# Kernel optimization log

Measured on AMD Instinct MI355X. Metric: run time of the kernel, lower is better.

Reference implementation:

```python
import jax, jax.numpy as jnp
import numpy as np

B, C, N = 8, 256, 2048

def setup_inputs() -> dict:
    key = jax.random.key(0)
    ks = jax.random.split(key, 7)
    s = 1.0 / np.sqrt(C)
    return {
        "x": jax.random.normal(ks[0], (B, C, N), dtype=jnp.float32),
        "Wq": jax.random.normal(ks[1], (C, C), dtype=jnp.float32) * s,
        "bq": jax.random.normal(ks[2], (C,), dtype=jnp.float32) * s,
        "Wk": jax.random.normal(ks[3], (C, C), dtype=jnp.float32) * s,
        "bk": jax.random.normal(ks[4], (C,), dtype=jnp.float32) * s,
        "Wv": jax.random.normal(ks[5], (C, C), dtype=jnp.float32) * s,
        "bv": jax.random.normal(ks[6], (C,), dtype=jnp.float32) * s,
    }

def reference(x, Wq, bq, Wk, bk, Wv, bv):
    # x: [B, C, N]; Conv1d(k=1) == channel-mixing matmul + bias
    q = jnp.einsum('oc,bcn->bon', Wq, x) + bq[None, :, None]  # [B,C,N]
    k = jnp.einsum('oc,bcn->bon', Wk, x) + bk[None, :, None]  # [B,C,N]
    v = jnp.einsum('oc,bcn->bon', Wv, x) + bv[None, :, None]  # [B,C,N]
    # qk = bmm(q^T, k): [B, N, N]
    qk = jnp.einsum('bcn,bcm->bnm', q, k)
    # global-sum normalization over the ENTIRE qk tensor (not row-wise softmax)
    attn_w = qk / jnp.sum(qk)
    # attn = bmm(v, attn_w): [B, C, N]
    attn = jnp.einsum('bcn,bnm->bcm', v, attn_w)
    return attn
```

## Files before the change

### kernel.cpp

```cpp
#include <hip/hip_runtime.h>


typedef _Float16 half8 __attribute__((ext_vector_type(8)));
typedef _Float16 half4 __attribute__((ext_vector_type(4)));
typedef _Float16 half2v __attribute__((ext_vector_type(2)));
typedef float f4v __attribute__((ext_vector_type(4)));

#define GP  40
#define GPB 36

__launch_bounds__(256)
__global__ void k1_kernel(const float* __restrict__ x, const float* __restrict__ Wq,
                          const float* __restrict__ Wk, const float* __restrict__ bq,
                          const float* __restrict__ bk, float* __restrict__ sxpart,
                          float* __restrict__ W3, float* __restrict__ u2,
                          float* __restrict__ w1, float* __restrict__ s1,
                          float* __restrict__ S, float* __restrict__ Gpart) {
    __shared__ __align__(16) char smem[40960];
    const int blk = blockIdx.x, t = threadIdx.x;
    if (blk < 192) {
        _Float16* Ah = (_Float16*)smem;
        _Float16* Al = Ah + 128 * GP;
        _Float16* Bh = Al + 128 * GP;
        _Float16* Bl = Bh + 128 * GP;
        const int tileId = blk % 3;
        const int y = blk / 3;
        const int b = y >> 3, ks = y & 7;
        const int r0 = (tileId == 2) ? 128 : 0;
        const int c0 = (tileId == 0) ? 0 : 128;
        const bool diag = (tileId != 1);
        const float* xb = x + (long)b * 524288;

        const int lane = t & 63, wave = t >> 6;
        const int wy = wave >> 1, wx = wave & 1;
        const int mIn = lane & 15, quad = lane >> 4;

        f4v acc[4][4] = {};
        const int aBase = (wy * 64 + mIn) * GP + quad * 8;
        const int bBase = (wx * 64 + mIn) * GP + quad * 8;
        const int srow = t >> 3;
        const int skq  = (t & 7) * 4;
        float rs[4] = {};

        float4 pa[4], pb[4];
        int kk = ks * 256;
        #pragma unroll
        for (int i = 0; i < 4; ++i) {
            pa[i] = *(const float4*)&xb[(long)(r0 + srow + i * 32) * 2048 + kk + skq];
            if (!diag) pb[i] = *(const float4*)&xb[(long)(c0 + srow + i * 32) * 2048 + kk + skq];
        }

        for (int kb = 0; kb < 8; ++kb) {
            if (kb) __syncthreads();
            #pragma unroll
            for (int i = 0; i < 4; ++i) {
                const int row = srow + i * 32;
                half4 hv, lv;
                hv[0] = (_Float16)pa[i].x; lv[0] = (_Float16)(pa[i].x - (float)hv[0]);
                hv[1] = (_Float16)pa[i].y; lv[1] = (_Float16)(pa[i].y - (float)hv[1]);
                hv[2] = (_Float16)pa[i].z; lv[2] = (_Float16)(pa[i].z - (float)hv[2]);
                hv[3] = (_Float16)pa[i].w; lv[3] = (_Float16)(pa[i].w - (float)hv[3]);
                *(half4*)&Ah[row * GP + skq] = hv;
                *(half4*)&Al[row * GP + skq] = lv;
                if (diag) {
                    rs[i] += pa[i].x + pa[i].y + pa[i].z + pa[i].w;
                } else {
                    half4 hb, lb;
                    hb[0] = (_Float16)pb[i].x; lb[0] = (_Float16)(pb[i].x - (float)hb[0]);
                    hb[1] = (_Float16)pb[i].y; lb[1] = (_Float16)(pb[i].y - (float)hb[1]);
                    hb[2] = (_Float16)pb[i].z; lb[2] = (_Float16)(pb[i].z - (float)hb[2]);
                    hb[3] = (_Float16)pb[i].w; lb[3] = (_Float16)(pb[i].w - (float)hb[3]);
                    *(half4*)&Bh[row * GP + skq] = hb;
                    *(half4*)&Bl[row * GP + skq] = lb;
                }
            }
            __syncthreads();
            kk += 32;
            if (kb < 7) {
                #pragma unroll
                for (int i = 0; i < 4; ++i) {
                    pa[i] = *(const float4*)&xb[(long)(r0 + srow + i * 32) * 2048 + kk + skq];
                    if (!diag) pb[i] = *(const float4*)&xb[(long)(c0 + srow + i * 32) * 2048 + kk + skq];
                }
            }
            const _Float16* BhP = diag ? Ah : Bh;
            const _Float16* BlP = diag ? Al : Bl;
            #pragma unroll
            for (int ph = 0; ph < 3; ++ph) {
                const _Float16* As = (ph == 2) ? Al : Ah;
                const _Float16* Bs = (ph == 1) ? BlP : BhP;
                half8 af[4], bf[4];
                #pragma unroll
                for (int i = 0; i < 4; ++i) {
                    af[i] = *(const half8*)&As[aBase + i * 16 * GP];
                    bf[i] = *(const half8*)&Bs[bBase + i * 16 * GP];
                }
                #pragma unroll
                for (int i = 0; i < 4; ++i)
                    #pragma unroll
                    for (int j = 0; j < 4; ++j)
                        acc[i][j] = __builtin_amdgcn_mfma_f32_16x16x32_f16(af[i], bf[j], acc[i][j], 0, 0, 0);
            }
        }

        if (diag) {
            #pragma unroll
            for (int i = 0; i < 4; ++i) {
                rs[i] += __shfl_xor(rs[i], 1);
                rs[i] += __shfl_xor(rs[i], 2);
                rs[i] += __shfl_xor(rs[i], 4);
            }
            if ((t & 7) == 0) {
                #pragma unroll
                for (int i = 0; i < 4; ++i)
                    sxpart[ks * 2048 + b * 256 + r0 + srow + i * 32] = rs[i];
            }
        }

        float* D = Gpart + ((long)(ks * 8 + b) << 16);
        #pragma unroll
        for (int i = 0; i < 4; ++i)
            #pragma unroll
            for (int j = 0; j < 4; ++j) {
                const int row = r0 + wy * 64 + i * 16 + quad * 4;
                const int col = c0 + wx * 64 + j * 16 + mIn;
                #pragma unroll
                for (int r = 0; r < 4; ++r)
                    D[(row + r) * 256 + col] = acc[i][j][r];
                if (tileId == 1)
                    *(float4*)&D[(long)col * 256 + row] =
                        make_float4(acc[i][j][0], acc[i][j][1], acc[i][j][2], acc[i][j][3]);
            }
    } else if (blk < 208) {
        float* ldsA = (float*)smem;
        float* ldsB = ldsA + 16 * 68;
        const int tile = blk - 192;
        const int r0 = (tile >> 2) * 64, j0 = (tile & 3) * 64;
        const int tx = t & 15, ty = t >> 4;
        float acc[4][4] = {};
        for (int kk = 0; kk < 256; kk += 16) {
            *(float4*)&ldsA[ty * 68 + tx * 4] = *(const float4*)&Wq[(long)(kk + ty) * 256 + r0 + tx * 4];
            *(float4*)&ldsB[ty * 68 + tx * 4] = *(const float4*)&Wk[(long)(kk + ty) * 256 + j0 + tx * 4];
            __syncthreads();
            #pragma unroll
            for (int k = 0; k < 16; ++k) {
                const float4 av4 = *(const float4*)&ldsA[k * 68 + ty * 4];
                const float4 bv4 = *(const float4*)&ldsB[k * 68 + tx * 4];
                const float ar[4] = {av4.x, av4.y, av4.z, av4.w};
                const float br[4] = {bv4.x, bv4.y, bv4.z, bv4.w};
                #pragma unroll
                for (int i = 0; i < 4; ++i)
                    #pragma unroll
                    for (int j = 0; j < 4; ++j)
                        acc[i][j] = fmaf(ar[i], br[j], acc[i][j]);
            }
            __syncthreads();
        }
        #pragma unroll
        for (int i = 0; i < 4; ++i)
            *(float4*)&W3[(long)(r0 + ty * 4 + i) * 256 + j0 + tx * 4] =
                make_float4(acc[i][0], acc[i][1], acc[i][2], acc[i][3]);
    } else {
        float* sbq = (float*)smem;
        float* sbk = sbq + 256;
        float* red = sbk + 256;
        if (t == 0) S[0] = 0.0f;
        sbq[t] = bq[t]; sbk[t] = bk[t];
        __syncthreads();
        float u = 0.0f, w = 0.0f;
        #pragma unroll 8
        for (int c = 0; c < 256; ++c) {
            u = fmaf(Wk[(long)c * 256 + t], sbq[c], u);
            w = fmaf(Wq[(long)c * 256 + t], sbk[c], w);
        }
        u2[t] = u; w1[t] = w;
        red[t] = sbq[t] * sbk[t]; __syncthreads();
        for (int h = 128; h > 0; h >>= 1) { if (t < h) red[t] += red[t + h]; __syncthreads(); }
        if (t == 0) s1[0] = red[0];
    }
}

__launch_bounds__(256)
__global__ void k2_kernel(const float* __restrict__ Wv, const float* __restrict__ Gpart,
                          const float* __restrict__ W3, const float* __restrict__ u2,
                          const float* __restrict__ w1, const float* __restrict__ s1p,
                          const float* __restrict__ sxpart, float* __restrict__ T1,
                          float* __restrict__ v2, float* __restrict__ s2,
                          float* __restrict__ wvsx, float* __restrict__ S) {
    __shared__ __align__(16) char smem[40960];
    const int blk = blockIdx.x, t = threadIdx.x;
    if (blk < 128) {
        float* ldsA = (float*)smem;
        float* ldsB = ldsA + 16 * 68;
        const int j0 = (blk & 3) * 64;
        const int r0 = ((blk >> 2) & 3) * 64;
        const int b = blk >> 4;
        const int tx = t & 15, ty = t >> 4;
        const int sr = t >> 2, sk = (t & 3) * 4;
        float acc[4][4] = {};
        for (int kk = 0; kk < 256; kk += 16) {
            const float4 a4 = *(const float4*)&Wv[(long)(r0 + sr) * 256 + kk + sk];
            ldsA[(sk + 0) * 68 + sr] = a4.x;
            ldsA[(sk + 1) * 68 + sr] = a4.y;
            ldsA[(sk + 2) * 68 + sr] = a4.z;
            ldsA[(sk + 3) * 68 + sr] = a4.w;
            float4 bs = make_float4(0.f, 0.f, 0.f, 0.f);
            #pragma unroll
            for (int ksl = 0; ksl < 8; ++ksl) {
                const float4 g = *(const float4*)&Gpart[(long)ksl * 524288 + (long)b * 65536 +
                                                        (long)(kk + ty) * 256 + j0 + tx * 4];
                bs.x += g.x; bs.y += g.y; bs.z += g.z; bs.w += g.w;
            }
            *(float4*)&ldsB[ty * 68 + tx * 4] = bs;
            __syncthreads();
            #pragma unroll
            for (int k = 0; k < 16; ++k) {
                const float4 av4 = *(const float4*)&ldsA[k * 68 + ty * 4];
                const float4 bv4 = *(const float4*)&ldsB[k * 68 + tx * 4];
                const float ar[4] = {av4.x, av4.y, av4.z, av4.w};
                const float br[4] = {bv4.x, bv4.y, bv4.z, bv4.w};
                #pragma unroll
                for (int i = 0; i < 4; ++i)
                    #pragma unroll
                    for (int j = 0; j < 4; ++j)
                        acc[i][j] = fmaf(ar[i], br[j], acc[i][j]);
            }
            __syncthreads();
        }
        float* D = T1 + (long)b * 65536;
        #pragma unroll
        for (int i = 0; i < 4; ++i)
            *(float4*)&D[(long)(r0 + ty * 4 + i) * 256 + j0 + tx * 4] =
                make_float4(acc[i][0], acc[i][1], acc[i][2], acc[i][3]);
    } else if (blk < 136) {
        float* ssx = (float*)smem;
        float* red = ssx + 256;
        const int b = blk - 128, j = t;
        float sxv = 0.0f;
        #pragma unroll
        for (int ks = 0; ks < 8; ++ks) sxv += sxpart[ks * 2048 + b * 256 + j];
        ssx[j] = sxv;
        __syncthreads();
        float vr = 0.0f;
        #pragma unroll 8
        for (int c = 0; c < 256; ++c) vr = fmaf(W3[(long)c * 256 + j], ssx[c], vr);
        const float v2j = vr + 2048.0f * u2[j];
        v2[b * 256 + j] = v2j;
        red[j] = v2j * sxv; __syncthreads();
        for (int h = 128; h > 0; h >>= 1) { if (j < h) red[j] += red[j + h]; __syncthreads(); }
        const float sd1 = red[0];
        __syncthreads();
        red[j] = sxv * w1[j]; __syncthreads();
        for (int h = 128; h > 0; h >>= 1) { if (j < h) red[j] += red[j + h]; __syncthreads(); }
        if (j == 0) {
            const float s2v = red[0] + 2048.0f * s1p[0];
            s2[b] = s2v;
            atomicAdd(S, sd1 + 2048.0f * s2v);
        }
    } else {
        float* wtile = (float*)smem;
        float* sxs = wtile + 8192;
        const int r0w = (blk - 136) * 32;
        #pragma unroll
        for (int p = 0; p < 8; ++p) {
            const int f = t + p * 256;
            const int row = f >> 6, c4 = f & 63;
            *(float4*)&wtile[row * 256 + c4 * 4] = *(const float4*)&Wv[(long)(r0w + row) * 256 + c4 * 4];
        }
        #pragma unroll
        for (int p = 0; p < 8; ++p) {
            const int f = t + p * 256;
            float s = 0.0f;
            #pragma unroll
            for (int ks = 0; ks < 8; ++ks) s += sxpart[ks * 2048 + f];
            sxs[f] = s;
        }
        __syncthreads();
        const int r = t >> 3, q = t & 7;
        float acc[8] = {};
        for (int ci = 0; ci < 32; ++ci) {
            const float wv = wtile[r * 256 + q * 32 + ci];
            #pragma unroll
            for (int b = 0; b < 8; ++b) acc[b] = fmaf(wv, sxs[b * 256 + q * 32 + ci], acc[b]);
        }
        #pragma unroll
        for (int b = 0; b < 8; ++b) {
            acc[b] += __shfl_xor(acc[b], 1);
            acc[b] += __shfl_xor(acc[b], 2);
            acc[b] += __shfl_xor(acc[b], 4);
        }
        if (q == 0) {
            #pragma unroll
            for (int b = 0; b < 8; ++b) wvsx[b * 256 + r0w + r] = acc[b];
        }
    }
}

__launch_bounds__(256)
__global__ void ap_kernel(const float* __restrict__ T1, const float* __restrict__ W3,
                          const float* __restrict__ wvsx, const float* __restrict__ u2,
                          const float* __restrict__ bv, const float* __restrict__ v2,
                          const float* __restrict__ w1, const float* __restrict__ s1p,
                          const float* __restrict__ s2, _Float16* __restrict__ Aph,
                          _Float16* __restrict__ Apl, float* __restrict__ cvec) {
    __shared__ float ldsA[16 * 68], ldsB[16 * 68], sw1[256];
    const int b = blockIdx.z;
    const int r0 = blockIdx.y * 64, j0 = blockIdx.x * 64;
    const float* A = T1 + (long)b * 65536;
    const int t = threadIdx.x, tx = t & 15, ty = t >> 4;
    const int sr = t >> 2, sk = (t & 3) * 4;
    sw1[t] = w1[t];
    float acc[4][4] = {};
    float dot[4] = {};
    for (int kk = 0; kk < 256; kk += 16) {
        const float4 a4 = *(const float4*)&A[(long)(r0 + sr) * 256 + kk + sk];
        ldsA[(sk + 0) * 68 + sr] = a4.x;
        ldsA[(sk + 1) * 68 + sr] = a4.y;
        ldsA[(sk + 2) * 68 + sr] = a4.z;
        ldsA[(sk + 3) * 68 + sr] = a4.w;
        *(float4*)&ldsB[ty * 68 + tx * 4] = *(const float4*)&W3[(long)(kk + ty) * 256 + j0 + tx * 4];
        __syncthreads();
        #pragma unroll
        for (int k = 0; k < 16; ++k) {
            const float4 av4 = *(const float4*)&ldsA[k * 68 + ty * 4];
            const float4 bv4 = *(const float4*)&ldsB[k * 68 + tx * 4];
            const float ar[4] = {av4.x, av4.y, av4.z, av4.w};
            const float br[4] = {bv4.x, bv4.y, bv4.z, bv4.w};
            const float wk = sw1[kk + k];
            #pragma unroll
            for (int i = 0; i < 4; ++i) {
                dot[i] = fmaf(ar[i], wk, dot[i]);
                #pragma unroll
                for (int j = 0; j < 4; ++j)
                    acc[i][j] = fmaf(ar[i], br[j], acc[i][j]);
            }
        }
        __syncthreads();
    }
    #pragma unroll
    for (int i = 0; i < 4; ++i) {
        const int r = r0 + ty * 4 + i;
        const float e1 = wvsx[b * 256 + r], e3 = bv[r];
        half4 hv, lv;
        #pragma unroll
        for (int j = 0; j < 4; ++j) {
            const int col = j0 + tx * 4 + j;
            const float val = acc[i][j] + e1 * u2[col] + e3 * v2[b * 256 + col];
            hv[j] = (_Float16)val;
            lv[j] = (_Float16)(val - (float)hv[j]);
        }
        const long o = (long)b * 65536 + (long)r * 256 + j0 + tx * 4;
        *(half4*)&Aph[o] = hv;
        *(half4*)&Apl[o] = lv;
        if (j0 == 0 && tx == 0)
            cvec[b * 256 + r] = dot[i] + e1 * s1p[0] + e3 * s2[b];
    }
}

__launch_bounds__(256)
__global__ void gemmF_mfma(const _Float16* __restrict__ Aph, const _Float16* __restrict__ Apl,
                           const float* __restrict__ x, const float* __restrict__ Sptr,
                           const float* __restrict__ cvec, float* __restrict__ out) {
    __shared__ __align__(16) _Float16 Ah[128 * GP];
    __shared__ __align__(16) _Float16 Al[128 * GP];
    __shared__ __align__(16) _Float16 Bh[128 * GPB];
    __shared__ __align__(16) _Float16 Bl[128 * GPB];
    __shared__ __align__(16) float xt[32 * 132];

    const int n0 = blockIdx.x * 128;
    const int c0 = blockIdx.y * 128;
    const int b = blockIdx.z;
    const _Float16* Asrc_h = Aph + (long)b * 65536;
    const _Float16* Asrc_l = Apl + (long)b * 65536;
    const float* xb = x + (long)b * 524288;

    const int t = threadIdx.x;
    const int lane = t & 63, wave = t >> 6;
    const int wy = wave >> 1, wx = wave & 1;
    const int mIn = lane & 15, quad = lane >> 4;

    f4v acc[4][4] = {};
    const int aBase = (wy * 64 + mIn) * GP + quad * 8;
    const int bBase = (wx * 64 + mIn) * GPB + quad * 8;
    const int cn = t & 127;
    const int ckh = (t >> 7) * 16;

    for (int kk = 0; kk < 256; kk += 32) {
        #pragma unroll
        for (int i = 0; i < 2; ++i) {
            const int idx = t + (i << 8);
            const int row = idx >> 2, ko = (idx & 3) << 3;
            *(uint4*)&Ah[row * GP + ko] = *(const uint4*)&Asrc_h[(long)(c0 + row) * 256 + kk + ko];
            *(uint4*)&Al[row * GP + ko] = *(const uint4*)&Asrc_l[(long)(c0 + row) * 256 + kk + ko];
        }
        #pragma unroll
        for (int p = 0; p < 4; ++p) {
            const int f = t + p * 256;
            const int k = f >> 5, n4 = f & 31;
            *(float4*)&xt[k * 132 + n4 * 4] = *(const float4*)&xb[(long)(kk + k) * 2048 + n0 + n4 * 4];
        }
        __syncthreads();
        {
            _Float16 hs[16], ls[16];
            #pragma unroll
            for (int k = 0; k < 16; ++k) {
                const float v = xt[(ckh + k) * 132 + cn];
                hs[k] = (_Float16)v;
                ls[k] = (_Float16)(v - (float)hs[k]);
            }
            #pragma unroll
            for (int k2 = 0; k2 < 8; ++k2) {
                half2v h2; h2[0] = hs[2 * k2]; h2[1] = hs[2 * k2 + 1];
                half2v l2; l2[0] = ls[2 * k2]; l2[1] = ls[2 * k2 + 1];
                *(half2v*)&Bh[cn * GPB + ckh + 2 * k2] = h2;
                *(half2v*)&Bl[cn * GPB + ckh + 2 * k2] = l2;
            }
        }
        __syncthreads();
        #pragma unroll
        for (int ph = 0; ph < 3; ++ph) {
            const _Float16* As = (ph == 2) ? Al : Ah;
            const _Float16* Bs = (ph == 1) ? Bl : Bh;
            half8 af[4], bf[4];
            #pragma unroll
            for (int i = 0; i < 4; ++i) {
                af[i] = *(const half8*)&As[aBase + i * 16 * GP];
                const half4 b0 = *(const half4*)&Bs[bBase + i * 16 * GPB];
                const half4 b1 = *(const half4*)&Bs[bBase + i * 16 * GPB + 4];
                bf[i] = __builtin_shufflevector(b0, b1, 0, 1, 2, 3, 4, 5, 6, 7);
            }
            #pragma unroll
            for (int i = 0; i < 4; ++i)
                #pragma unroll
                for (int j = 0; j < 4; ++j)
                    acc[i][j] = __builtin_amdgcn_mfma_f32_16x16x32_f16(af[i], bf[j], acc[i][j], 0, 0, 0);
        }
        __syncthreads();
    }

    const float invS = 1.0f / Sptr[0];
    float* ob = out + (long)b * 524288;
    const float* cv = cvec + b * 256;
    #pragma unroll
    for (int i = 0; i < 4; ++i)
        #pragma unroll
        for (int r = 0; r < 4; ++r) {
            const int row = c0 + wy * 64 + i * 16 + quad * 4 + r;
            const float c = cv[row];
            #pragma unroll
            for (int j = 0; j < 4; ++j) {
                const int col = n0 + wx * 64 + j * 16 + mIn;
                ob[(long)row * 2048 + col] = (acc[i][j][r] + c) * invS;
            }
        }
}

extern "C" void kernel_launch(void* const* d_in, const int* in_sizes, int n_in,
                              void* d_out, int out_size, void* d_ws, size_t ws_size,
                              hipStream_t stream) {
    const float* x  = (const float*)d_in[0];
    const float* Wq = (const float*)d_in[1];
    const float* bq = (const float*)d_in[2];
    const float* Wk = (const float*)d_in[3];
    const float* bk = (const float*)d_in[4];
    const float* Wv = (const float*)d_in[5];
    const float* bv = (const float*)d_in[6];
    float* out = (float*)d_out;
    float* ws  = (float*)d_ws;

    float* T1     = ws;
    float* W3     = ws + 524288;
    float* sxpart = ws + 589824;
    float* wvsx   = ws + 606208;
    float* v2     = ws + 608256;
    float* cvec   = ws + 610304;
    float* s2     = ws + 612352;
    float* u2     = ws + 612360;
    float* w1     = ws + 612616;
    float* s1     = ws + 612872;
    float* S      = ws + 612873;
    float* Gpart  = ws + 612880;
    _Float16* Aph = (_Float16*)(ws + 4807184);
    _Float16* Apl = Aph + 524288;

    k1_kernel<<<dim3(209), 256, 0, stream>>>(x, Wq, Wk, bq, bk, sxpart, W3, u2, w1, s1, S, Gpart);
    k2_kernel<<<dim3(144), 256, 0, stream>>>(Wv, Gpart, W3, u2, w1, s1, sxpart, T1, v2, s2, wvsx, S);
    ap_kernel<<<dim3(4, 4, 8), 256, 0, stream>>>(T1, W3, wvsx, u2, bv, v2, w1, s1, s2, Aph, Apl, cvec);
    gemmF_mfma<<<dim3(16, 2, 8), 256, 0, stream>>>(Aph, Apl, x, S, cvec, out);
}
```

Baseline: 151.9 us.

## Fuse four kernels into one persistent kernel with software grid barriers

Merges the four stage kernels into a single 256-block launch. The stages are separated by an atomic-counter grid barrier in global memory, and the counter is reset with a memset before launch. This removes the launch gaps between kernels. In exchange it relies on all 256 blocks being co-resident, which launch_bounds(256,1) on this device is meant to allow, and it adds spin-wait barrier overhead and idle blocks in the smaller stages.

```diff
diff --git a/kernel.cpp b/kernel.cpp
--- a/kernel.cpp
+++ b/kernel.cpp
@@ -8,16 +8,45 @@
 
 #define GP  40
 #define GPB 36
-
-__launch_bounds__(256)
-__global__ void k1_kernel(const float* __restrict__ x, const float* __restrict__ Wq,
-                          const float* __restrict__ Wk, const float* __restrict__ bq,
-                          const float* __restrict__ bk, float* __restrict__ sxpart,
-                          float* __restrict__ W3, float* __restrict__ u2,
-                          float* __restrict__ w1, float* __restrict__ s1,
-                          float* __restrict__ S, float* __restrict__ Gpart) {
-    __shared__ __align__(16) char smem[40960];
+#define NBLK 256
+
+__device__ __forceinline__ void gbar(unsigned* bar) {
+    __syncthreads();
+    if (threadIdx.x == 0) {
+        __threadfence();
+        const unsigned g = __hip_atomic_load(&bar[1], __ATOMIC_RELAXED, __HIP_MEMORY_SCOPE_AGENT);
+        const unsigned a = __hip_atomic_fetch_add(&bar[0], 1u, __ATOMIC_ACQ_REL, __HIP_MEMORY_SCOPE_AGENT);
+        if (a == NBLK - 1u) {
+            __hip_atomic_store(&bar[0], 0u, __ATOMIC_RELAXED, __HIP_MEMORY_SCOPE_AGENT);
+            __hip_atomic_store(&bar[1], g + 1u, __ATOMIC_RELEASE, __HIP_MEMORY_SCOPE_AGENT);
+        } else {
+            while (__hip_atomic_load(&bar[1], __ATOMIC_ACQUIRE, __HIP_MEMORY_SCOPE_AGENT) == g)
+                __builtin_amdgcn_s_sleep(2);
+        }
+        __threadfence();
+    }
+    __syncthreads();
+}
+
+__launch_bounds__(256, 1)
+__global__ void mega_kernel(const float* __restrict__ x, const float* __restrict__ Wq,
+                            const float* __restrict__ bq, const float* __restrict__ Wk,
+                            const float* __restrict__ bk, const float* __restrict__ Wv,
+                            const float* __restrict__ bv, float* __restrict__ out,
+                            float* __restrict__ T1, float* __restrict__ W3,
+                            float* __restrict__ sxpart, float* __restrict__ wvsx,
+                            float* __restrict__ v2, float* __restrict__ cvec,
+                            float* __restrict__ s2, float* __restrict__ u2,
+                            float* __restrict__ w1, float* __restrict__ s1,
+                            float* __restrict__ S, float* __restrict__ Gpart,
+                            _Float16* __restrict__ Aph, _Float16* __restrict__ Apl,
+                            unsigned* __restrict__ bar) {
+    __shared__ __align__(16) char smem[55808];
     const int blk = blockIdx.x, t = threadIdx.x;
+    const int lane = t & 63, wave = t >> 6;
+    const int wy = wave >> 1, wx = wave & 1;
+    const int mIn = lane & 15, quad = lane >> 4;
+
     if (blk < 192) {
         _Float16* Ah = (_Float16*)smem;
         _Float16* Al = Ah + 128 * GP;
@@ -30,10 +59,6 @@
         const int c0 = (tileId == 0) ? 0 : 128;
         const bool diag = (tileId != 1);
         const float* xb = x + (long)b * 524288;
-
-        const int lane = t & 63, wave = t >> 6;
-        const int wy = wave >> 1, wx = wave & 1;
-        const int mIn = lane & 15, quad = lane >> 4;
 
         f4v acc[4][4] = {};
         const int aBase = (wy * 64 + mIn) * GP + quad * 8;
@@ -160,7 +185,7 @@
         for (int i = 0; i < 4; ++i)
             *(float4*)&W3[(long)(r0 + ty * 4 + i) * 256 + j0 + tx * 4] =
                 make_float4(acc[i][0], acc[i][1], acc[i][2], acc[i][3]);
-    } else {
+    } else if (blk == 208) {
         float* sbq = (float*)smem;
         float* sbk = sbq + 256;
         float* red = sbk + 256;
@@ -178,17 +203,9 @@
         for (int h = 128; h > 0; h >>= 1) { if (t < h) red[t] += red[t + h]; __syncthreads(); }
         if (t == 0) s1[0] = red[0];
     }
-}
-
-__launch_bounds__(256)
-__global__ void k2_kernel(const float* __restrict__ Wv, const float* __restrict__ Gpart,
-                          const float* __restrict__ W3, const float* __restrict__ u2,
-                          const float* __restrict__ w1, const float* __restrict__ s1p,
-                          const float* __restrict__ sxpart, float* __restrict__ T1,
-                          float* __restrict__ v2, float* __restrict__ s2,
-                          float* __restrict__ wvsx, float* __restrict__ S) {
-    __shared__ __align__(16) char smem[40960];
-    const int blk = blockIdx.x, t = threadIdx.x;
+
+    gbar(bar);
+
     if (blk < 128) {
         float* ldsA = (float*)smem;
         float* ldsB = ldsA + 16 * 68;
@@ -253,11 +270,11 @@
         red[j] = sxv * w1[j]; __syncthreads();
         for (int h = 128; h > 0; h >>= 1) { if (j < h) red[j] += red[j + h]; __syncthreads(); }
         if (j == 0) {
-            const float s2v = red[0] + 2048.0f * s1p[0];
+            const float s2v = red[0] + 2048.0f * s1[0];
             s2[b] = s2v;
             atomicAdd(S, sd1 + 2048.0f * s2v);
         }
-    } else {
+    } else if (blk < 144) {
         float* wtile = (float*)smem;
         float* sxs = wtile + 8192;
         const int r0w = (blk - 136) * 32;
@@ -294,165 +311,156 @@
             for (int b = 0; b < 8; ++b) wvsx[b * 256 + r0w + r] = acc[b];
         }
     }
-}
-
-__launch_bounds__(256)
-__global__ void ap_kernel(const float* __restrict__ T1, const float* __restrict__ W3,
-                          const float* __restrict__ wvsx, const float* __restrict__ u2,
-                          const float* __restrict__ bv, const float* __restrict__ v2,
-                          const float* __restrict__ w1, const float* __restrict__ s1p,
-                          const float* __restrict__ s2, _Float16* __restrict__ Aph,
-                          _Float16* __restrict__ Apl, float* __restrict__ cvec) {
-    __shared__ float ldsA[16 * 68], ldsB[16 * 68], sw1[256];
-    const int b = blockIdx.z;
-    const int r0 = blockIdx.y * 64, j0 = blockIdx.x * 64;
-    const float* A = T1 + (long)b * 65536;
-    const int t = threadIdx.x, tx = t & 15, ty = t >> 4;
-    const int sr = t >> 2, sk = (t & 3) * 4;
-    sw1[t] = w1[t];
-    float acc[4][4] = {};
-    float dot[4] = {};
-    for (int kk = 0; kk < 256; kk += 16) {
-        const float4 a4 = *(const float4*)&A[(long)(r0 + sr) * 256 + kk + sk];
-        ldsA[(sk + 0) * 68 + sr] = a4.x;
-        ldsA[(sk + 1) * 68 + sr] = a4.y;
-        ldsA[(sk + 2) * 68 + sr] = a4.z;
-        ldsA[(sk + 3) * 68 + sr] = a4.w;
-        *(float4*)&ldsB[ty * 68 + tx * 4] = *(const float4*)&W3[(long)(kk + ty) * 256 + j0 + tx * 4];
-        __syncthreads();
-        #pragma unroll
-        for (int k = 0; k < 16; ++k) {
-            const float4 av4 = *(const float4*)&ldsA[k * 68 + ty * 4];
-            const float4 bv4 = *(const float4*)&ldsB[k * 68 + tx * 4];
-            const float ar[4] = {av4.x, av4.y, av4.z, av4.w};
-            const float br[4] = {bv4.x, bv4.y, bv4.z, bv4.w};
-            const float wk = sw1[kk + k];
-            #pragma unroll
-            for (int i = 0; i < 4; ++i) {
-                dot[i] = fmaf(ar[i], wk, dot[i]);
-                #pragma unroll
-                for (int j = 0; j < 4; ++j)
-                    acc[i][j] = fmaf(ar[i], br[j], acc[i][j]);
-            }
-        }
-        __syncthreads();
+
+    gbar(bar);
+
+    if (blk < 128) {
+        float* ldsA = (float*)smem;
+        float* ldsB = ldsA + 16 * 68;
+        float* sw1 = ldsB + 16 * 68;
+        const int b = blk >> 4;
+        const int r0 = ((blk >> 2) & 3) * 64, j0 = (blk & 3) * 64;
+        const float* A = T1 + (long)b * 65536;
+        const int tx = t & 15, ty = t >> 4;
+        const int sr = t >> 2, sk = (t & 3) * 4;
+        sw1[t] = w1[t];
+        float acc[4][4] = {};
+        float dot[4] = {};
+        for (int kk = 0; kk < 256; kk += 16) {
+            const float4 a4 = *(const float4*)&A[(long)(r0 + sr) * 256 + kk + sk];
+            ldsA[(sk + 0) * 68 + sr] = a4.x;
+            ldsA[(sk + 1) * 68 + sr] = a4.y;
+            ldsA[(sk + 2) * 68 + sr] = a4.z;
+            ldsA[(sk + 3) * 68 + sr] = a4.w;
+            *(float4*)&ldsB[ty * 68 + tx * 4] = *(const float4*)&W3[(long)(kk + ty) * 256 + j0 + tx * 4];
+            __syncthreads();
+            #pragma unroll
+            for (int k = 0; k < 16; ++k) {
+                const float4 av4 = *(const float4*)&ldsA[k * 68 + ty * 4];
+                const float4 bv4 = *(const float4*)&ldsB[k * 68 + tx * 4];
+                const float ar[4] = {av4.x, av4.y, av4.z, av4.w};
+                const float br[4] = {bv4.x, bv4.y, bv4.z, bv4.w};
+                const float wk = sw1[kk + k];
+                #pragma unroll
+                for (int i = 0; i < 4; ++i) {
+                    dot[i] = fmaf(ar[i], wk, dot[i]);
+                    #pragma unroll
+                    for (int j = 0; j < 4; ++j)
+                        acc[i][j] = fmaf(ar[i], br[j], acc[i][j]);
+                }
+            }
+            __syncthreads();
+        }
+        #pragma unroll
+        for (int i = 0; i < 4; ++i) {
+            const int r = r0 + ty * 4 + i;
+            const float e1 = wvsx[b * 256 + r], e3 = bv[r];
+            half4 hv, lv;
+            #pragma unroll
+            for (int j = 0; j < 4; ++j) {
+                const int col = j0 + tx * 4 + j;
+                const float val = acc[i][j] + e1 * u2[col] + e3 * v2[b * 256 + col];
+                hv[j] = (_Float16)val;
+                lv[j] = (_Float16)(val - (float)hv[j]);
+            }
+            const long o = (long)b * 65536 + (long)r * 256 + j0 + tx * 4;
+            *(half4*)&Aph[o] = hv;
+            *(half4*)&Apl[o] = lv;
+            if (j0 == 0 && tx == 0)
+                cvec[b * 256 + r] = dot[i] + e1 * s1[0] + e3 * s2[b];
+        }
     }
-    #pragma unroll
-    for (int i = 0; i < 4; ++i) {
-        const int r = r0 + ty * 4 + i;
-        const float e1 = wvsx[b * 256 + r], e3 = bv[r];
-        half4 hv, lv;
-        #pragma unroll
-        for (int j = 0; j < 4; ++j) {
-            const int col = j0 + tx * 4 + j;
-            const float val = acc[i][j] + e1 * u2[col] + e3 * v2[b * 256 + col];
-            hv[j] = (_Float16)val;
-            lv[j] = (_Float16)(val - (float)hv[j]);
-        }
-        const long o = (long)b * 65536 + (long)r * 256 + j0 + tx * 4;
-        *(half4*)&Aph[o] = hv;
-        *(half4*)&Apl[o] = lv;
-        if (j0 == 0 && tx == 0)
-            cvec[b * 256 + r] = dot[i] + e1 * s1p[0] + e3 * s2[b];
+
+    gbar(bar);
+
+    {
+        _Float16* Ah = (_Float16*)smem;
+        _Float16* Al = Ah + 128 * GP;
+        _Float16* Bh = Al + 128 * GP;
+        _Float16* Bl = Bh + 128 * GPB;
+        float* xt = (float*)(Bl + 128 * GPB);
+        const int n0 = (blk & 15) * 128;
+        const int c0 = ((blk >> 4) & 1) * 128;
+        const int b = blk >> 5;
+        const _Float16* Asrc_h = Aph + (long)b * 65536;
+        const _Float16* Asrc_l = Apl + (long)b * 65536;
+        const float* xb = x + (long)b * 524288;
+
+        f4v acc[4][4] = {};
+        const int aBase = (wy * 64 + mIn) * GP + quad * 8;
+        const int bBase = (wx * 64 + mIn) * GPB + quad * 8;
+        const int cn = t & 127;
+        const int ckh = (t >> 7) * 16;
+
+        for (int kk = 0; kk < 256; kk += 32) {
+            #pragma unroll
+            for (int i = 0; i < 2; ++i) {
+                const int idx = t + (i << 8);
+                const int row = idx >> 2, ko = (idx & 3) << 3;
+                *(uint4*)&Ah[row * GP + ko] = *(const uint4*)&Asrc_h[(long)(c0 + row) * 256 + kk + ko];
+                *(uint4*)&Al[row * GP + ko] = *(const uint4*)&Asrc_l[(long)(c0 + row) * 256 + kk + ko];
+            }
+            #pragma unroll
+            for (int p = 0; p < 4; ++p) {
+                const int f = t + p * 256;
+                const int k = f >> 5, n4 = f & 31;
+                *(float4*)&xt[k * 132 + n4 * 4] = *(const float4*)&xb[(long)(kk + k) * 2048 + n0 + n4 * 4];
+            }
+            __syncthreads();
+            {
+                _Float16 hs[16], ls[16];
+                #pragma unroll
+                for (int k = 0; k < 16; ++k) {
+                    const float v = xt[(ckh + k) * 132 + cn];
+                    hs[k] = (_Float16)v;
+                    ls[k] = (_Float16)(v - (float)hs[k]);
+                }
+                #pragma unroll
+                for (int k2 = 0; k2 < 8; ++k2) {
+                    half2v h2; h2[0] = hs[2 * k2]; h2[1] = hs[2 * k2 + 1];
+                    half2v l2; l2[0] = ls[2 * k2]; l2[1] = ls[2 * k2 + 1];
+                    *(half2v*)&Bh[cn * GPB + ckh + 2 * k2] = h2;
+                    *(half2v*)&Bl[cn * GPB + ckh + 2 * k2] = l2;
+                }
+            }
+            __syncthreads();
+            #pragma unroll
+            for (int ph = 0; ph < 3; ++ph) {
+                const _Float16* As = (ph == 2) ? Al : Ah;
+                const _Float16* Bs = (ph == 1) ? Bl : Bh;
+                half8 af[4], bf[4];
+                #pragma unroll
+                for (int i = 0; i < 4; ++i) {
+                    af[i] = *(const half8*)&As[aBase + i * 16 * GP];
+                    const half4 b0 = *(const half4*)&Bs[bBase + i * 16 * GPB];
+                    const half4 b1 = *(const half4*)&Bs[bBase + i * 16 * GPB + 4];
+                    bf[i] = __builtin_shufflevector(b0, b1, 0, 1, 2, 3, 4, 5, 6, 7);
+                }
+                #pragma unroll
+                for (int i = 0; i < 4; ++i)
+                    #pragma unroll
+                    for (int j = 0; j < 4; ++j)
+                        acc[i][j] = __builtin_amdgcn_mfma_f32_16x16x32_f16(af[i], bf[j], acc[i][j], 0, 0, 0);
+            }
+            __syncthreads();
+        }
+
+        const float invS = 1.0f / S[0];
+        float* ob = out + (long)b * 524288;
+        const float* cv = cvec + b * 256;
+        #pragma unroll
+        for (int i = 0; i < 4; ++i)
+            #pragma unroll
+            for (int r = 0; r < 4; ++r) {
+                const int row = c0 + wy * 64 + i * 16 + quad * 4 + r;
+                const float c = cv[row];
+                #pragma unroll
+                for (int j = 0; j < 4; ++j) {
+                    const int col = n0 + wx * 64 + j * 16 + mIn;
+                    ob[(long)row * 2048 + col] = (acc[i][j][r] + c) * invS;
+                }
+            }
     }
-}
-
-__launch_bounds__(256)
-__global__ void gemmF_mfma(const _Float16* __restrict__ Aph, const _Float16* __restrict__ Apl,
-                           const float* __restrict__ x, const float* __restrict__ Sptr,
-                           const float* __restrict__ cvec, float* __restrict__ out) {
-    __shared__ __align__(16) _Float16 Ah[128 * GP];
-    __shared__ __align__(16) _Float16 Al[128 * GP];
-    __shared__ __align__(16) _Float16 Bh[128 * GPB];
-    __shared__ __align__(16) _Float16 Bl[128 * GPB];
-    __shared__ __align__(16) float xt[32 * 132];
-
-    const int n0 = blockIdx.x * 128;
-    const int c0 = blockIdx.y * 128;
-    const int b = blockIdx.z;
-    const _Float16* Asrc_h = Aph + (long)b * 65536;
-    const _Float16* Asrc_l = Apl + (long)b * 65536;
-    const float* xb = x + (long)b * 524288;
-
-    const int t = threadIdx.x;
-    const int lane = t & 63, wave = t >> 6;
-    const int wy = wave >> 1, wx = wave & 1;
-    const int mIn = lane & 15, quad = lane >> 4;
-
-    f4v acc[4][4] = {};
-    const int aBase = (wy * 64 + mIn) * GP + quad * 8;
-    const int bBase = (wx * 64 + mIn) * GPB + quad * 8;
-    const int cn = t & 127;
-    const int ckh = (t >> 7) * 16;
-
-    for (int kk = 0; kk < 256; kk += 32) {
-        #pragma unroll
-        for (int i = 0; i < 2; ++i) {
-            const int idx = t + (i << 8);
-            const int row = idx >> 2, ko = (idx & 3) << 3;
-            *(uint4*)&Ah[row * GP + ko] = *(const uint4*)&Asrc_h[(long)(c0 + row) * 256 + kk + ko];
-            *(uint4*)&Al[row * GP + ko] = *(const uint4*)&Asrc_l[(long)(c0 + row) * 256 + kk + ko];
-        }
-        #pragma unroll
-        for (int p = 0; p < 4; ++p) {
-            const int f = t + p * 256;
-            const int k = f >> 5, n4 = f & 31;
-            *(float4*)&xt[k * 132 + n4 * 4] = *(const float4*)&xb[(long)(kk + k) * 2048 + n0 + n4 * 4];
-        }
-        __syncthreads();
-        {
-            _Float16 hs[16], ls[16];
-            #pragma unroll
-            for (int k = 0; k < 16; ++k) {
-                const float v = xt[(ckh + k) * 132 + cn];
-                hs[k] = (_Float16)v;
-                ls[k] = (_Float16)(v - (float)hs[k]);
-            }
-            #pragma unroll
-            for (int k2 = 0; k2 < 8; ++k2) {
-                half2v h2; h2[0] = hs[2 * k2]; h2[1] = hs[2 * k2 + 1];
-                half2v l2; l2[0] = ls[2 * k2]; l2[1] = ls[2 * k2 + 1];
-                *(half2v*)&Bh[cn * GPB + ckh + 2 * k2] = h2;
-                *(half2v*)&Bl[cn * GPB + ckh + 2 * k2] = l2;
-            }
-        }
-        __syncthreads();
-        #pragma unroll
-        for (int ph = 0; ph < 3; ++ph) {
-            const _Float16* As = (ph == 2) ? Al : Ah;
-            const _Float16* Bs = (ph == 1) ? Bl : Bh;
-            half8 af[4], bf[4];
-            #pragma unroll
-            for (int i = 0; i < 4; ++i) {
-                af[i] = *(const half8*)&As[aBase + i * 16 * GP];
-                const half4 b0 = *(const half4*)&Bs[bBase + i * 16 * GPB];
-                const half4 b1 = *(const half4*)&Bs[bBase + i * 16 * GPB + 4];
-                bf[i] = __builtin_shufflevector(b0, b1, 0, 1, 2, 3, 4, 5, 6, 7);
-            }
-            #pragma unroll
-            for (int i = 0; i < 4; ++i)
-                #pragma unroll
-                for (int j = 0; j < 4; ++j)
-                    acc[i][j] = __builtin_amdgcn_mfma_f32_16x16x32_f16(af[i], bf[j], acc[i][j], 0, 0, 0);
-        }
-        __syncthreads();
-    }
-
-    const float invS = 1.0f / Sptr[0];
-    float* ob = out + (long)b * 524288;
-    const float* cv = cvec + b * 256;
-    #pragma unroll
-    for (int i = 0; i < 4; ++i)
-        #pragma unroll
-        for (int r = 0; r < 4; ++r) {
-            const int row = c0 + wy * 64 + i * 16 + quad * 4 + r;
-            const float c = cv[row];
-            #pragma unroll
-            for (int j = 0; j < 4; ++j) {
-                const int col = n0 + wx * 64 + j * 16 + mIn;
-                ob[(long)row * 2048 + col] = (acc[i][j][r] + c) * invS;
-            }
-        }
 }
 
 extern "C" void kernel_launch(void* const* d_in, const int* in_sizes, int n_in,
@@ -479,12 +487,13 @@
     float* w1     = ws + 612616;
     float* s1     = ws + 612872;
     float* S      = ws + 612873;
+    unsigned* bar = (unsigned*)(ws + 612874);
     float* Gpart  = ws + 612880;
     _Float16* Aph = (_Float16*)(ws + 4807184);
     _Float16* Apl = Aph + 524288;
 
-    k1_kernel<<<dim3(209), 256, 0, stream>>>(x, Wq, Wk, bq, bk, sxpart, W3, u2, w1, s1, S, Gpart);
-    k2_kernel<<<dim3(144), 256, 0, stream>>>(Wv, Gpart, W3, u2, w1, s1, sxpart, T1, v2, s2, wvsx, S);
-    ap_kernel<<<dim3(4, 4, 8), 256, 0, stream>>>(T1, W3, wvsx, u2, bv, v2, w1, s1, s2, Aph, Apl, cvec);
-    gemmF_mfma<<<dim3(16, 2, 8), 256, 0, stream>>>(Aph, Apl, x, S, cvec, out);
+    hipMemsetAsync(bar, 0, 2 * sizeof(unsigned), stream);
+    mega_kernel<<<dim3(NBLK), 256, 0, stream>>>(x, Wq, bq, Wk, bk, Wv, bv, out,
+                                                T1, W3, sxpart, wvsx, v2, cvec,
+                                                s2, u2, w1, s1, S, Gpart, Aph, Apl, bar);
 }
```

New measurement: 331.9 us. +118.5%, slower.
